# Kernel tuning notes

Hardware: AMD Instinct MI355X
Metric: run time of the kernel (lower is better)

Reference implementation:

```python
import jax, jax.numpy as jnp
import numpy as np

N = 100000
E = 1280000
D = 64


def setup_inputs() -> dict:
    key = jax.random.key(0)
    k1, k2, k3, k4, k5, k6 = jax.random.split(key, 6)
    return {
        "x": jax.random.normal(k1, (N, D), dtype=jnp.float32),
        "w_src": jax.random.normal(k2, (D,), dtype=jnp.float32),
        "w_dst": jax.random.normal(k3, (D,), dtype=jnp.float32),
        "ew": jax.random.normal(k4, (E,), dtype=jnp.float32),
        "src_idx": jax.random.randint(k5, (E,), 0, N, dtype=jnp.int64),
        "dst_idx": jax.random.randint(k6, (E,), 0, N, dtype=jnp.int64),
    }


def reference(x, w_src, w_dst, ew, src_idx, dst_idx):
    # Per-node scalar scores: Linear(emb_dim, 1, bias=False)
    a_src = x @ w_src            # [N]
    a_dst = x @ w_dst            # [N]
    # Edge attention: tanh(a_src[u] + a_dst[v]) * ew  (u_add_v + tanh + scale)
    a = jnp.tanh(a_src[src_idx] + a_dst[dst_idx]) * ew   # [E]
    # Message = a_e * x[src_e]; reduce = scatter-sum over dst (u_mul_e + sum)
    m = a[:, None] * x[src_idx]                           # [E, D]
    h = jax.ops.segment_sum(m, dst_idx, num_segments=N)   # [N, D]
    return h
```

## Files before the change

kernel.cpp:

```cpp
#include <hip/hip_runtime.h>
#include <hip/hip_fp16.h>
#include <math.h>

#define DIM  64
#define SPAN 256
#define SPAN_SHIFT 8
#define NBIN 256
#define KMAX 512
#define CAP  6144

__global__ void score_kernel(const float* __restrict__ x,
                             const float* __restrict__ w_src,
                             const float* __restrict__ w_dst,
                             float* __restrict__ a_src,
                             float* __restrict__ a_dst,
                             __half* __restrict__ xh,
                             int N) {
    int gid  = blockIdx.x * blockDim.x + threadIdx.x;
    int node = gid >> 6;
    int lane = threadIdx.x & 63;
    if (node >= N) return;
    float xv = x[(size_t)node * DIM + lane];
    xh[(size_t)node * DIM + lane] = __float2half_rn(xv);
    float s1 = xv * w_src[lane];
    float s2 = xv * w_dst[lane];
    #pragma unroll
    for (int off = 32; off > 0; off >>= 1) {
        s1 += __shfl_down(s1, off, 64);
        s2 += __shfl_down(s2, off, 64);
    }
    if (lane == 0) {
        a_src[node] = s1;
        a_dst[node] = s2;
    }
}

__global__ __launch_bounds__(1024) void hist_coarse(
        const int* __restrict__ dst, int* __restrict__ cnt,
        int E, int N, int K) {
    __shared__ int lh[KMAX];
    int tid = threadIdx.x;
    for (int j = tid; j < K; j += blockDim.x) lh[j] = 0;
    __syncthreads();
    for (int base = blockIdx.x * 1024; base < E; base += NBIN * 1024) {
        int e = base + tid;
        if (e < E) {
            unsigned t = (unsigned)dst[e];
            if (t >= (unsigned)N) t = 0;
            atomicAdd(&lh[t >> SPAN_SHIFT], 1);
        }
    }
    __syncthreads();
    for (int j = tid; j < K; j += blockDim.x)
        cnt[j * NBIN + blockIdx.x] = lh[j];
}

__global__ void scan_part(const int* __restrict__ cnt, int* __restrict__ offs,
                          int* __restrict__ bsum, int N) {
    __shared__ int buf[2][256];
    int tid = threadIdx.x;
    int i = blockIdx.x * 256 + tid;
    int v = (i < N) ? cnt[i] : 0;
    int sel = 0;
    buf[0][tid] = v;
    __syncthreads();
    for (int off = 1; off < 256; off <<= 1) {
        int nsel = sel ^ 1;
        buf[nsel][tid] = buf[sel][tid] + ((tid >= off) ? buf[sel][tid - off] : 0);
        __syncthreads();
        sel = nsel;
    }
    if (i < N) offs[i] = buf[sel][tid] - v;
    if (tid == 255) bsum[blockIdx.x] = buf[sel][255];
}

__global__ void scan_top(int* __restrict__ bsum, int* __restrict__ offs,
                         int NB, int N) {
    __shared__ int buf[2][512];
    int tid = threadIdx.x;
    int v = (tid < NB) ? bsum[tid] : 0;
    int sel = 0;
    buf[0][tid] = v;
    __syncthreads();
    for (int off = 1; off < 512; off <<= 1) {
        int nsel = sel ^ 1;
        buf[nsel][tid] = buf[sel][tid] + ((tid >= off) ? buf[sel][tid - off] : 0);
        __syncthreads();
        sel = nsel;
    }
    if (tid < NB) bsum[tid] = buf[sel][tid] - v;
    if (tid == 511) offs[N] = buf[sel][511];
}

__global__ __launch_bounds__(1024) void binpass_kernel(
        const float* __restrict__ ew,
        const int* __restrict__ src_idx,
        const int* __restrict__ dst_idx,
        const float* __restrict__ a_src,
        const float* __restrict__ a_dst,
        const int* __restrict__ moffs,
        const int* __restrict__ bsum,
        unsigned long long* __restrict__ pay,
        int E, int N, int K) {
    __shared__ int lcur[KMAX];
    int tid = threadIdx.x;
    for (int j = tid; j < K; j += blockDim.x) {
        int i = j * NBIN + blockIdx.x;
        lcur[j] = moffs[i] + bsum[i >> 8];
    }
    __syncthreads();
    for (int base = blockIdx.x * 1024; base < E; base += NBIN * 1024) {
        int e = base + tid;
        if (e < E) {
            unsigned s = (unsigned)src_idx[e];
            unsigned t = (unsigned)dst_idx[e];
            if (s >= (unsigned)N) s = 0;
            if (t >= (unsigned)N) t = 0;
            float a = tanhf(a_src[s] + a_dst[t]) * ew[e];
            int bk = (int)(t >> SPAN_SHIFT);
            int pos = atomicAdd(&lcur[bk], 1);
            unsigned rec = (s << 8) | (t & (SPAN - 1u));
            pay[pos] = ((unsigned long long)rec << 32) |
                       (unsigned long long)__float_as_uint(a);
        }
    }
}

__global__ __launch_bounds__(1024) void sort_gather_kernel(
        const __half* __restrict__ xh,
        const float* __restrict__ x32,
        const unsigned long long* __restrict__ pay,
        const int* __restrict__ moffs,
        const int* __restrict__ bsum,
        float* __restrict__ h,
        int N, int K, int E) {
    __shared__ unsigned long long srec[CAP];
    __shared__ unsigned short sidx[CAP];
    __shared__ int hcnt[SPAN];
    __shared__ int hoff[2][SPAN];
    __shared__ int lcur[SPAN];
    __shared__ int nstart[SPAN];
    int tid = threadIdx.x;
    int b   = blockIdx.x;
    int i0 = b * NBIN;
    int bstart = moffs[i0] + bsum[i0 >> 8];
    int bend;
    if (b == K - 1) bend = E;
    else { int i1 = (b + 1) * NBIN; bend = moffs[i1] + bsum[i1 >> 8]; }
    int cnt = bend - bstart;

    if (cnt <= CAP) {
        if (tid < SPAN) hcnt[tid] = 0;
        __syncthreads();
        for (int i = tid; i < cnt; i += 1024) {
            unsigned long long r = pay[bstart + i];
            srec[i] = r;
            atomicAdd(&hcnt[(int)((r >> 32) & (SPAN - 1u))], 1);
        }
        __syncthreads();
        int sel = 0;
        if (tid < SPAN) hoff[0][tid] = hcnt[tid];
        __syncthreads();
        for (int off = 1; off < SPAN; off <<= 1) {
            int nsel = sel ^ 1;
            if (tid < SPAN)
                hoff[nsel][tid] = hoff[sel][tid] +
                                  ((tid >= off) ? hoff[sel][tid - off] : 0);
            __syncthreads();
            sel = nsel;
        }
        if (tid < SPAN) {
            int excl = hoff[sel][tid] - hcnt[tid];
            nstart[tid] = excl;
            lcur[tid]   = excl;
        }
        __syncthreads();
        for (int i = tid; i < cnt; i += 1024) {
            unsigned long long r = srec[i];
            int d = (int)((r >> 32) & (SPAN - 1u));
            int pos = atomicAdd(&lcur[d], 1);
            sidx[pos] = (unsigned short)i;
        }
        __syncthreads();
        int lane = tid & 63;
        int wave = tid >> 6;
        int grp  = lane >> 4;
        int sub  = lane & 15;
        for (int d0 = (wave << 2); d0 < SPAN; d0 += 64) {
            int d = d0 + grp;
            int node = b * SPAN + d;
            int p  = nstart[d];
            int pe = p + hcnt[d];
            if (node >= N) pe = p;
            float ax = 0.f, ay = 0.f, az = 0.f, aw = 0.f;
            while (p + 4 <= pe) {
                unsigned long long r0 = srec[sidx[p]];
                unsigned long long r1 = srec[sidx[p + 1]];
                unsigned long long r2 = srec[sidx[p + 2]];
                unsigned long long r3 = srec[sidx[p + 3]];
                p += 4;
                unsigned s0 = (unsigned)(r0 >> 40); if (s0 >= (unsigned)N) s0 = 0;
                unsigned s1 = (unsigned)(r1 >> 40); if (s1 >= (unsigned)N) s1 = 0;
                unsigned s2 = (unsigned)(r2 >> 40); if (s2 >= (unsigned)N) s2 = 0;
                unsigned s3 = (unsigned)(r3 >> 40); if (s3 >= (unsigned)N) s3 = 0;
                uint2 v0 = *(const uint2*)(xh + (size_t)s0 * DIM + (sub << 2));
                uint2 v1 = *(const uint2*)(xh + (size_t)s1 * DIM + (sub << 2));
                uint2 v2 = *(const uint2*)(xh + (size_t)s2 * DIM + (sub << 2));
                uint2 v3 = *(const uint2*)(xh + (size_t)s3 * DIM + (sub << 2));
                float a0 = __uint_as_float((unsigned)r0);
                float a1 = __uint_as_float((unsigned)r1);
                float a2 = __uint_as_float((unsigned)r2);
                float a3 = __uint_as_float((unsigned)r3);
                float2 lo0 = __half22float2(*(const __half2*)&v0.x);
                float2 hi0 = __half22float2(*(const __half2*)&v0.y);
                float2 lo1 = __half22float2(*(const __half2*)&v1.x);
                float2 hi1 = __half22float2(*(const __half2*)&v1.y);
                float2 lo2 = __half22float2(*(const __half2*)&v2.x);
                float2 hi2 = __half22float2(*(const __half2*)&v2.y);
                float2 lo3 = __half22float2(*(const __half2*)&v3.x);
                float2 hi3 = __half22float2(*(const __half2*)&v3.y);
                ax = fmaf(a0, lo0.x, ax); ay = fmaf(a0, lo0.y, ay);
                az = fmaf(a0, hi0.x, az); aw = fmaf(a0, hi0.y, aw);
                ax = fmaf(a1, lo1.x, ax); ay = fmaf(a1, lo1.y, ay);
                az = fmaf(a1, hi1.x, az); aw = fmaf(a1, hi1.y, aw);
                ax = fmaf(a2, lo2.x, ax); ay = fmaf(a2, lo2.y, ay);
                az = fmaf(a2, hi2.x, az); aw = fmaf(a2, hi2.y, aw);
                ax = fmaf(a3, lo3.x, ax); ay = fmaf(a3, lo3.y, ay);
                az = fmaf(a3, hi3.x, az); aw = fmaf(a3, hi3.y, aw);
            }
            if (p < pe) {
                int q1 = p + 1, q2 = p + 2, q3 = p + 3;
                unsigned long long r0 = srec[sidx[p]];
                unsigned long long r1 = (q1 < pe) ? srec[sidx[q1]] : 0ULL;
                unsigned long long r2 = (q2 < pe) ? srec[sidx[q2]] : 0ULL;
                unsigned long long r3 = (q3 < pe) ? srec[sidx[q3]] : 0ULL;
                unsigned s0 = (unsigned)(r0 >> 40); if (s0 >= (unsigned)N) s0 = 0;
                unsigned s1 = (unsigned)(r1 >> 40); if (s1 >= (unsigned)N) s1 = 0;
                unsigned s2 = (unsigned)(r2 >> 40); if (s2 >= (unsigned)N) s2 = 0;
                unsigned s3 = (unsigned)(r3 >> 40); if (s3 >= (unsigned)N) s3 = 0;
                uint2 v0 = *(const uint2*)(xh + (size_t)s0 * DIM + (sub << 2));
                uint2 v1 = *(const uint2*)(xh + (size_t)s1 * DIM + (sub << 2));
                uint2 v2 = *(const uint2*)(xh + (size_t)s2 * DIM + (sub << 2));
                uint2 v3 = *(const uint2*)(xh + (size_t)s3 * DIM + (sub << 2));
                float a0 = __uint_as_float((unsigned)r0);
                float a1 = __uint_as_float((unsigned)r1);
                float a2 = __uint_as_float((unsigned)r2);
                float a3 = __uint_as_float((unsigned)r3);
                float2 lo0 = __half22float2(*(const __half2*)&v0.x);
                float2 hi0 = __half22float2(*(const __half2*)&v0.y);
                float2 lo1 = __half22float2(*(const __half2*)&v1.x);
                float2 hi1 = __half22float2(*(const __half2*)&v1.y);
                float2 lo2 = __half22float2(*(const __half2*)&v2.x);
                float2 hi2 = __half22float2(*(const __half2*)&v2.y);
                float2 lo3 = __half22float2(*(const __half2*)&v3.x);
                float2 hi3 = __half22float2(*(const __half2*)&v3.y);
                ax = fmaf(a0, lo0.x, ax); ay = fmaf(a0, lo0.y, ay);
                az = fmaf(a0, hi0.x, az); aw = fmaf(a0, hi0.y, aw);
                ax = fmaf(a1, lo1.x, ax); ay = fmaf(a1, lo1.y, ay);
                az = fmaf(a1, hi1.x, az); aw = fmaf(a1, hi1.y, aw);
                ax = fmaf(a2, lo2.x, ax); ay = fmaf(a2, lo2.y, ay);
                az = fmaf(a2, hi2.x, az); aw = fmaf(a2, hi2.y, aw);
                ax = fmaf(a3, lo3.x, ax); ay = fmaf(a3, lo3.y, ay);
                az = fmaf(a3, hi3.x, az); aw = fmaf(a3, hi3.y, aw);
            }
            if (node < N) {
                *(float4*)(h + (size_t)node * DIM + (sub << 2)) =
                    make_float4(ax, ay, az, aw);
            }
        }
    } else {
        for (int j = tid; j < SPAN * DIM; j += 1024) {
            int node = b * SPAN + (j >> 6);
            if (node < N) h[(size_t)node * DIM + (j & 63)] = 0.f;
        }
        __syncthreads();
        for (int i = tid; i < cnt; i += 1024) {
            unsigned long long r = pay[bstart + i];
            unsigned s = (unsigned)(r >> 40);
            if (s >= (unsigned)N) s = 0;
            int node = b * SPAN + (int)((r >> 32) & (SPAN - 1u));
            float a = __uint_as_float((unsigned)r);
            if (node < N)
                for (int k = 0; k < DIM; ++k)
                    atomicAdd(&h[(size_t)node * DIM + k],
                              a * x32[(size_t)s * DIM + k]);
        }
    }
}

__global__ void zero_h_kernel(float* __restrict__ p, int n) {
    int i = blockIdx.x * blockDim.x + threadIdx.x;
    if (i < n) p[i] = 0.f;
}

__global__ void edge_kernel_atomic(const float* __restrict__ x,
                                   const float* __restrict__ ew,
                                   const int* __restrict__ src_idx,
                                   const int* __restrict__ dst_idx,
                                   const float* __restrict__ a_src,
                                   const float* __restrict__ a_dst,
                                   float* __restrict__ h,
                                   int E) {
    int gid  = blockIdx.x * blockDim.x + threadIdx.x;
    int e    = gid >> 6;
    int lane = threadIdx.x & 63;
    if (e >= E) return;
    int s = src_idx[e];
    int t = dst_idx[e];
    float a  = tanhf(a_src[s] + a_dst[t]) * ew[e];
    float xv = x[(size_t)s * DIM + lane];
    atomicAdd(&h[(size_t)t * DIM + lane], a * xv);
}

__global__ void score_only_kernel(const float* __restrict__ x,
                                  const float* __restrict__ w_src,
                                  const float* __restrict__ w_dst,
                                  float* __restrict__ a_src,
                                  float* __restrict__ a_dst,
                                  int N) {
    int gid  = blockIdx.x * blockDim.x + threadIdx.x;
    int node = gid >> 6;
    int lane = threadIdx.x & 63;
    if (node >= N) return;
    float xv = x[(size_t)node * DIM + lane];
    float s1 = xv * w_src[lane];
    float s2 = xv * w_dst[lane];
    #pragma unroll
    for (int off = 32; off > 0; off >>= 1) {
        s1 += __shfl_down(s1, off, 64);
        s2 += __shfl_down(s2, off, 64);
    }
    if (lane == 0) {
        a_src[node] = s1;
        a_dst[node] = s2;
    }
}

extern "C" void kernel_launch(void* const* d_in, const int* in_sizes, int n_in,
                              void* d_out, int out_size, void* d_ws, size_t ws_size,
                              hipStream_t stream) {
    const float* x     = (const float*)d_in[0];
    const float* w_src = (const float*)d_in[1];
    const float* w_dst = (const float*)d_in[2];
    const float* ew    = (const float*)d_in[3];
    const int*   src   = (const int*)d_in[4];
    const int*   dst   = (const int*)d_in[5];
    float* h = (float*)d_out;

    int N = in_sizes[0] / DIM;
    int E = in_sizes[3];

    int K    = (N + SPAN - 1) / SPAN;
    int Ntot = K * NBIN;
    int NBs  = (Ntot + 255) / 256;

    float* a_src  = (float*)d_ws;
    float* a_dst  = a_src + N;
    int*   moffs  = (int*)(a_dst + N);
    int*   bsum   = moffs + Ntot + 1;
    size_t head_bytes = ((size_t)(2 * N) + (size_t)Ntot + 1 + (size_t)NBs) * 4;
    size_t pay_off = (head_bytes + 15) & ~(size_t)15;
    unsigned long long* pay = (unsigned long long*)((char*)d_ws + pay_off);
    size_t xh_off = pay_off + (size_t)E * 8;
    __half* xh = (__half*)((char*)d_ws + xh_off);
    size_t need = xh_off + (size_t)N * DIM * 2;

    int score_blocks = (N + 3) / 4;

    if (ws_size < need || K > KMAX || NBs > 512 || (N * DIM) % 2 != 0) {
        score_only_kernel<<<score_blocks, 256, 0, stream>>>(x, w_src, w_dst,
                                                            a_src, a_dst, N);
        int ob = (out_size + 255) / 256;
        zero_h_kernel<<<ob, 256, 0, stream>>>(h, out_size);
        int edge_blocks = (E + 3) / 4;
        edge_kernel_atomic<<<edge_blocks, 256, 0, stream>>>(x, ew, src, dst,
                                                            a_src, a_dst, h, E);
        return;
    }

    score_kernel<<<score_blocks, 256, 0, stream>>>(x, w_src, w_dst,
                                                   a_src, a_dst, xh, N);
    hist_coarse<<<NBIN, 1024, 0, stream>>>(dst, moffs, E, N, K);
    scan_part<<<NBs, 256, 0, stream>>>(moffs, moffs, bsum, Ntot);
    scan_top<<<1, 512, 0, stream>>>(bsum, moffs, NBs, Ntot);
    binpass_kernel<<<NBIN, 1024, 0, stream>>>(ew, src, dst, a_src, a_dst,
                                              moffs, bsum, pay, E, N, K);
    sort_gather_kernel<<<K, 1024, 0, stream>>>(xh, x, pay, moffs, bsum,
                                               h, N, K, E);
}
```

Before: 179.5 us.

## Fuse score, histogram, scan, binning and gather into one cooperative kernel

```diff
diff --git a/kernel.cpp b/kernel.cpp
--- a/kernel.cpp
+++ b/kernel.cpp
@@ -1,117 +1,114 @@
 #include <hip/hip_runtime.h>
+#include <hip/hip_cooperative_groups.h>
 #include <hip/hip_fp16.h>
 #include <math.h>
+
+namespace cg = cooperative_groups;
+typedef unsigned long long ull;
 
 #define DIM  64
 #define SPAN 256
 #define SPAN_SHIFT 8
-#define NBIN 256
 #define KMAX 512
 #define CAP  6144
-
-__global__ void score_kernel(const float* __restrict__ x,
-                             const float* __restrict__ w_src,
-                             const float* __restrict__ w_dst,
-                             float* __restrict__ a_src,
-                             float* __restrict__ a_dst,
-                             __half* __restrict__ xh,
-                             int N) {
-    int gid  = blockIdx.x * blockDim.x + threadIdx.x;
-    int node = gid >> 6;
-    int lane = threadIdx.x & 63;
-    if (node >= N) return;
-    float xv = x[(size_t)node * DIM + lane];
-    xh[(size_t)node * DIM + lane] = __float2half_rn(xv);
-    float s1 = xv * w_src[lane];
-    float s2 = xv * w_dst[lane];
-    #pragma unroll
-    for (int off = 32; off > 0; off >>= 1) {
-        s1 += __shfl_down(s1, off, 64);
-        s2 += __shfl_down(s2, off, 64);
-    }
-    if (lane == 0) {
-        a_src[node] = s1;
-        a_dst[node] = s2;
-    }
-}
-
-__global__ __launch_bounds__(1024) void hist_coarse(
-        const int* __restrict__ dst, int* __restrict__ cnt,
-        int E, int N, int K) {
-    __shared__ int lh[KMAX];
-    int tid = threadIdx.x;
-    for (int j = tid; j < K; j += blockDim.x) lh[j] = 0;
-    __syncthreads();
-    for (int base = blockIdx.x * 1024; base < E; base += NBIN * 1024) {
-        int e = base + tid;
-        if (e < E) {
-            unsigned t = (unsigned)dst[e];
-            if (t >= (unsigned)N) t = 0;
-            atomicAdd(&lh[t >> SPAN_SHIFT], 1);
-        }
-    }
-    __syncthreads();
-    for (int j = tid; j < K; j += blockDim.x)
-        cnt[j * NBIN + blockIdx.x] = lh[j];
-}
-
-__global__ void scan_part(const int* __restrict__ cnt, int* __restrict__ offs,
-                          int* __restrict__ bsum, int N) {
-    __shared__ int buf[2][256];
-    int tid = threadIdx.x;
-    int i = blockIdx.x * 256 + tid;
-    int v = (i < N) ? cnt[i] : 0;
-    int sel = 0;
-    buf[0][tid] = v;
-    __syncthreads();
-    for (int off = 1; off < 256; off <<= 1) {
-        int nsel = sel ^ 1;
-        buf[nsel][tid] = buf[sel][tid] + ((tid >= off) ? buf[sel][tid - off] : 0);
-        __syncthreads();
-        sel = nsel;
-    }
-    if (i < N) offs[i] = buf[sel][tid] - v;
-    if (tid == 255) bsum[blockIdx.x] = buf[sel][255];
-}
-
-__global__ void scan_top(int* __restrict__ bsum, int* __restrict__ offs,
-                         int NB, int N) {
-    __shared__ int buf[2][512];
-    int tid = threadIdx.x;
-    int v = (tid < NB) ? bsum[tid] : 0;
-    int sel = 0;
-    buf[0][tid] = v;
-    __syncthreads();
-    for (int off = 1; off < 512; off <<= 1) {
-        int nsel = sel ^ 1;
-        buf[nsel][tid] = buf[sel][tid] + ((tid >= off) ? buf[sel][tid - off] : 0);
-        __syncthreads();
-        sel = nsel;
-    }
-    if (tid < NB) bsum[tid] = buf[sel][tid] - v;
-    if (tid == 511) offs[N] = buf[sel][511];
-}
-
-__global__ __launch_bounds__(1024) void binpass_kernel(
+#define TPB  1024
+#define GRID 256
+
+#define SMEM_BYTES 66560
+
+__global__ __launch_bounds__(TPB) void fused_kernel(
+        const float* __restrict__ x,
+        const float* __restrict__ w_src,
+        const float* __restrict__ w_dst,
         const float* __restrict__ ew,
         const int* __restrict__ src_idx,
         const int* __restrict__ dst_idx,
-        const float* __restrict__ a_src,
-        const float* __restrict__ a_dst,
-        const int* __restrict__ moffs,
-        const int* __restrict__ bsum,
-        unsigned long long* __restrict__ pay,
-        int E, int N, int K) {
-    __shared__ int lcur[KMAX];
-    int tid = threadIdx.x;
-    for (int j = tid; j < K; j += blockDim.x) {
-        int i = j * NBIN + blockIdx.x;
-        lcur[j] = moffs[i] + bsum[i >> 8];
-    }
-    __syncthreads();
-    for (int base = blockIdx.x * 1024; base < E; base += NBIN * 1024) {
-        int e = base + tid;
-        if (e < E) {
+        float* __restrict__ a_src,
+        float* __restrict__ a_dst,
+        __half* __restrict__ xh,
+        int* __restrict__ moffs,
+        int* __restrict__ bsum,
+        ull* __restrict__ pay,
+        float* __restrict__ h,
+        int N, int E, int K, int NBs) {
+    cg::grid_group grid = cg::this_grid();
+    const int G   = gridDim.x;
+    const int b   = blockIdx.x;
+    const int tid = threadIdx.x;
+    __shared__ __align__(16) char smem[SMEM_BYTES];
+
+    {
+        int* lh = (int*)smem;
+        for (int j = tid; j < K; j += TPB) lh[j] = 0;
+        __syncthreads();
+        int lane = tid & 63;
+        for (int node = b * 16 + (tid >> 6); node < N; node += G * 16) {
+            float xv = x[(size_t)node * DIM + lane];
+            xh[(size_t)node * DIM + lane] = __float2half_rn(xv);
+            float s1 = xv * w_src[lane];
+            float s2 = xv * w_dst[lane];
+            #pragma unroll
+            for (int off = 32; off > 0; off >>= 1) {
+                s1 += __shfl_down(s1, off, 64);
+                s2 += __shfl_down(s2, off, 64);
+            }
+            if (lane == 0) { a_src[node] = s1; a_dst[node] = s2; }
+        }
+        for (int e = b * TPB + tid; e < E; e += G * TPB) {
+            unsigned t = (unsigned)dst_idx[e];
+            if (t >= (unsigned)N) t = 0;
+            atomicAdd(&lh[t >> SPAN_SHIFT], 1);
+        }
+        __syncthreads();
+        for (int j = tid; j < K; j += TPB) moffs[j * G + b] = lh[j];
+    }
+    grid.sync();
+
+    int Ntot = K * G;
+    if (b < NBs) {
+        int* buf = (int*)smem;
+        int i = b * TPB + tid;
+        int v = (i < Ntot) ? moffs[i] : 0;
+        int sel = 0;
+        buf[tid] = v;
+        __syncthreads();
+        for (int off = 1; off < TPB; off <<= 1) {
+            int nsel = sel ^ 1;
+            int add = (tid >= off) ? buf[sel * TPB + tid - off] : 0;
+            buf[nsel * TPB + tid] = buf[sel * TPB + tid] + add;
+            __syncthreads();
+            sel = nsel;
+        }
+        if (i < Ntot) moffs[i] = buf[sel * TPB + tid] - v;
+        if (tid == TPB - 1) bsum[b] = buf[sel * TPB + tid];
+    }
+    grid.sync();
+
+    if (b == 0) {
+        int* buf = (int*)smem;
+        int v = (tid < NBs) ? bsum[tid] : 0;
+        int sel = 0;
+        buf[tid] = v;
+        __syncthreads();
+        for (int off = 1; off < TPB; off <<= 1) {
+            int nsel = sel ^ 1;
+            int add = (tid >= off) ? buf[sel * TPB + tid - off] : 0;
+            buf[nsel * TPB + tid] = buf[sel * TPB + tid] + add;
+            __syncthreads();
+            sel = nsel;
+        }
+        if (tid < NBs) bsum[tid] = buf[sel * TPB + tid] - v;
+    }
+    grid.sync();
+
+    {
+        int* lcur = (int*)smem;
+        for (int j = tid; j < K; j += TPB) {
+            int i = j * G + b;
+            lcur[j] = moffs[i] + bsum[i >> 10];
+        }
+        __syncthreads();
+        for (int e = b * TPB + tid; e < E; e += G * TPB) {
             unsigned s = (unsigned)src_idx[e];
             unsigned t = (unsigned)dst_idx[e];
             if (s >= (unsigned)N) s = 0;
@@ -120,170 +117,163 @@
             int bk = (int)(t >> SPAN_SHIFT);
             int pos = atomicAdd(&lcur[bk], 1);
             unsigned rec = (s << 8) | (t & (SPAN - 1u));
-            pay[pos] = ((unsigned long long)rec << 32) |
-                       (unsigned long long)__float_as_uint(a);
-        }
-    }
-}
-
-__global__ __launch_bounds__(1024) void sort_gather_kernel(
-        const __half* __restrict__ xh,
-        const float* __restrict__ x32,
-        const unsigned long long* __restrict__ pay,
-        const int* __restrict__ moffs,
-        const int* __restrict__ bsum,
-        float* __restrict__ h,
-        int N, int K, int E) {
-    __shared__ unsigned long long srec[CAP];
-    __shared__ unsigned short sidx[CAP];
-    __shared__ int hcnt[SPAN];
-    __shared__ int hoff[2][SPAN];
-    __shared__ int lcur[SPAN];
-    __shared__ int nstart[SPAN];
-    int tid = threadIdx.x;
-    int b   = blockIdx.x;
-    int i0 = b * NBIN;
-    int bstart = moffs[i0] + bsum[i0 >> 8];
-    int bend;
-    if (b == K - 1) bend = E;
-    else { int i1 = (b + 1) * NBIN; bend = moffs[i1] + bsum[i1 >> 8]; }
-    int cnt = bend - bstart;
-
-    if (cnt <= CAP) {
-        if (tid < SPAN) hcnt[tid] = 0;
-        __syncthreads();
-        for (int i = tid; i < cnt; i += 1024) {
-            unsigned long long r = pay[bstart + i];
-            srec[i] = r;
-            atomicAdd(&hcnt[(int)((r >> 32) & (SPAN - 1u))], 1);
-        }
-        __syncthreads();
-        int sel = 0;
-        if (tid < SPAN) hoff[0][tid] = hcnt[tid];
-        __syncthreads();
-        for (int off = 1; off < SPAN; off <<= 1) {
-            int nsel = sel ^ 1;
-            if (tid < SPAN)
-                hoff[nsel][tid] = hoff[sel][tid] +
-                                  ((tid >= off) ? hoff[sel][tid - off] : 0);
-            __syncthreads();
-            sel = nsel;
-        }
-        if (tid < SPAN) {
-            int excl = hoff[sel][tid] - hcnt[tid];
-            nstart[tid] = excl;
-            lcur[tid]   = excl;
-        }
-        __syncthreads();
-        for (int i = tid; i < cnt; i += 1024) {
-            unsigned long long r = srec[i];
-            int d = (int)((r >> 32) & (SPAN - 1u));
-            int pos = atomicAdd(&lcur[d], 1);
-            sidx[pos] = (unsigned short)i;
-        }
-        __syncthreads();
-        int lane = tid & 63;
-        int wave = tid >> 6;
-        int grp  = lane >> 4;
-        int sub  = lane & 15;
-        for (int d0 = (wave << 2); d0 < SPAN; d0 += 64) {
-            int d = d0 + grp;
-            int node = b * SPAN + d;
-            int p  = nstart[d];
-            int pe = p + hcnt[d];
-            if (node >= N) pe = p;
-            float ax = 0.f, ay = 0.f, az = 0.f, aw = 0.f;
-            while (p + 4 <= pe) {
-                unsigned long long r0 = srec[sidx[p]];
-                unsigned long long r1 = srec[sidx[p + 1]];
-                unsigned long long r2 = srec[sidx[p + 2]];
-                unsigned long long r3 = srec[sidx[p + 3]];
-                p += 4;
-                unsigned s0 = (unsigned)(r0 >> 40); if (s0 >= (unsigned)N) s0 = 0;
-                unsigned s1 = (unsigned)(r1 >> 40); if (s1 >= (unsigned)N) s1 = 0;
-                unsigned s2 = (unsigned)(r2 >> 40); if (s2 >= (unsigned)N) s2 = 0;
-                unsigned s3 = (unsigned)(r3 >> 40); if (s3 >= (unsigned)N) s3 = 0;
-                uint2 v0 = *(const uint2*)(xh + (size_t)s0 * DIM + (sub << 2));
-                uint2 v1 = *(const uint2*)(xh + (size_t)s1 * DIM + (sub << 2));
-                uint2 v2 = *(const uint2*)(xh + (size_t)s2 * DIM + (sub << 2));
-                uint2 v3 = *(const uint2*)(xh + (size_t)s3 * DIM + (sub << 2));
-                float a0 = __uint_as_float((unsigned)r0);
-                float a1 = __uint_as_float((unsigned)r1);
-                float a2 = __uint_as_float((unsigned)r2);
-                float a3 = __uint_as_float((unsigned)r3);
-                float2 lo0 = __half22float2(*(const __half2*)&v0.x);
-                float2 hi0 = __half22float2(*(const __half2*)&v0.y);
-                float2 lo1 = __half22float2(*(const __half2*)&v1.x);
-                float2 hi1 = __half22float2(*(const __half2*)&v1.y);
-                float2 lo2 = __half22float2(*(const __half2*)&v2.x);
-                float2 hi2 = __half22float2(*(const __half2*)&v2.y);
-                float2 lo3 = __half22float2(*(const __half2*)&v3.x);
-                float2 hi3 = __half22float2(*(const __half2*)&v3.y);
-                ax = fmaf(a0, lo0.x, ax); ay = fmaf(a0, lo0.y, ay);
-                az = fmaf(a0, hi0.x, az); aw = fmaf(a0, hi0.y, aw);
-                ax = fmaf(a1, lo1.x, ax); ay = fmaf(a1, lo1.y, ay);
-                az = fmaf(a1, hi1.x, az); aw = fmaf(a1, hi1.y, aw);
-                ax = fmaf(a2, lo2.x, ax); ay = fmaf(a2, lo2.y, ay);
-                az = fmaf(a2, hi2.x, az); aw = fmaf(a2, hi2.y, aw);
-                ax = fmaf(a3, lo3.x, ax); ay = fmaf(a3, lo3.y, ay);
-                az = fmaf(a3, hi3.x, az); aw = fmaf(a3, hi3.y, aw);
-            }
-            if (p < pe) {
-                int q1 = p + 1, q2 = p + 2, q3 = p + 3;
-                unsigned long long r0 = srec[sidx[p]];
-                unsigned long long r1 = (q1 < pe) ? srec[sidx[q1]] : 0ULL;
-                unsigned long long r2 = (q2 < pe) ? srec[sidx[q2]] : 0ULL;
-                unsigned long long r3 = (q3 < pe) ? srec[sidx[q3]] : 0ULL;
-                unsigned s0 = (unsigned)(r0 >> 40); if (s0 >= (unsigned)N) s0 = 0;
-                unsigned s1 = (unsigned)(r1 >> 40); if (s1 >= (unsigned)N) s1 = 0;
-                unsigned s2 = (unsigned)(r2 >> 40); if (s2 >= (unsigned)N) s2 = 0;
-                unsigned s3 = (unsigned)(r3 >> 40); if (s3 >= (unsigned)N) s3 = 0;
-                uint2 v0 = *(const uint2*)(xh + (size_t)s0 * DIM + (sub << 2));
-                uint2 v1 = *(const uint2*)(xh + (size_t)s1 * DIM + (sub << 2));
-                uint2 v2 = *(const uint2*)(xh + (size_t)s2 * DIM + (sub << 2));
-                uint2 v3 = *(const uint2*)(xh + (size_t)s3 * DIM + (sub << 2));
-                float a0 = __uint_as_float((unsigned)r0);
-                float a1 = __uint_as_float((unsigned)r1);
-                float a2 = __uint_as_float((unsigned)r2);
-                float a3 = __uint_as_float((unsigned)r3);
-                float2 lo0 = __half22float2(*(const __half2*)&v0.x);
-                float2 hi0 = __half22float2(*(const __half2*)&v0.y);
-                float2 lo1 = __half22float2(*(const __half2*)&v1.x);
-                float2 hi1 = __half22float2(*(const __half2*)&v1.y);
-                float2 lo2 = __half22float2(*(const __half2*)&v2.x);
-                float2 hi2 = __half22float2(*(const __half2*)&v2.y);
-                float2 lo3 = __half22float2(*(const __half2*)&v3.x);
-                float2 hi3 = __half22float2(*(const __half2*)&v3.y);
-                ax = fmaf(a0, lo0.x, ax); ay = fmaf(a0, lo0.y, ay);
-                az = fmaf(a0, hi0.x, az); aw = fmaf(a0, hi0.y, aw);
-                ax = fmaf(a1, lo1.x, ax); ay = fmaf(a1, lo1.y, ay);
-                az = fmaf(a1, hi1.x, az); aw = fmaf(a1, hi1.y, aw);
-                ax = fmaf(a2, lo2.x, ax); ay = fmaf(a2, lo2.y, ay);
-                az = fmaf(a2, hi2.x, az); aw = fmaf(a2, hi2.y, aw);
-                ax = fmaf(a3, lo3.x, ax); ay = fmaf(a3, lo3.y, ay);
-                az = fmaf(a3, hi3.x, az); aw = fmaf(a3, hi3.y, aw);
-            }
-            if (node < N) {
-                *(float4*)(h + (size_t)node * DIM + (sub << 2)) =
-                    make_float4(ax, ay, az, aw);
-            }
-        }
-    } else {
-        for (int j = tid; j < SPAN * DIM; j += 1024) {
-            int node = b * SPAN + (j >> 6);
-            if (node < N) h[(size_t)node * DIM + (j & 63)] = 0.f;
-        }
-        __syncthreads();
-        for (int i = tid; i < cnt; i += 1024) {
-            unsigned long long r = pay[bstart + i];
-            unsigned s = (unsigned)(r >> 40);
-            if (s >= (unsigned)N) s = 0;
-            int node = b * SPAN + (int)((r >> 32) & (SPAN - 1u));
-            float a = __uint_as_float((unsigned)r);
-            if (node < N)
-                for (int k = 0; k < DIM; ++k)
-                    atomicAdd(&h[(size_t)node * DIM + k],
-                              a * x32[(size_t)s * DIM + k]);
+            pay[pos] = ((ull)rec << 32) | (ull)__float_as_uint(a);
+        }
+    }
+    grid.sync();
+
+    ull* srec            = (ull*)smem;
+    unsigned short* sidx = (unsigned short*)(smem + CAP * 8);
+    int* hcnt            = (int*)(smem + CAP * 8 + CAP * 2);
+    int* hoff            = (int*)(smem + CAP * 8 + CAP * 2 + SPAN * 4);
+    int* lcur4           = (int*)(smem + CAP * 8 + CAP * 2 + SPAN * 4 * 3);
+    int* nstart          = (int*)(smem + CAP * 8 + CAP * 2 + SPAN * 4 * 4);
+
+    for (int bkt = b; bkt < K; bkt += G) {
+        __syncthreads();
+        int i0 = bkt * G;
+        int bstart = moffs[i0] + bsum[i0 >> 10];
+        int bend;
+        if (bkt == K - 1) bend = E;
+        else { int i1 = (bkt + 1) * G; bend = moffs[i1] + bsum[i1 >> 10]; }
+        int cnt = bend - bstart;
+
+        if (cnt <= CAP) {
+            if (tid < SPAN) hcnt[tid] = 0;
+            __syncthreads();
+            for (int i = tid; i < cnt; i += TPB) {
+                ull r = pay[bstart + i];
+                srec[i] = r;
+                atomicAdd(&hcnt[(int)((r >> 32) & (SPAN - 1u))], 1);
+            }
+            __syncthreads();
+            int sel = 0;
+            if (tid < SPAN) hoff[tid] = hcnt[tid];
+            __syncthreads();
+            for (int off = 1; off < SPAN; off <<= 1) {
+                int nsel = sel ^ 1;
+                if (tid < SPAN)
+                    hoff[nsel * SPAN + tid] = hoff[sel * SPAN + tid] +
+                        ((tid >= off) ? hoff[sel * SPAN + tid - off] : 0);
+                __syncthreads();
+                sel = nsel;
+            }
+            if (tid < SPAN) {
+                int excl = hoff[sel * SPAN + tid] - hcnt[tid];
+                nstart[tid] = excl;
+                lcur4[tid]  = excl;
+            }
+            __syncthreads();
+            for (int i = tid; i < cnt; i += TPB) {
+                ull r = srec[i];
+                int d = (int)((r >> 32) & (SPAN - 1u));
+                int pos = atomicAdd(&lcur4[d], 1);
+                sidx[pos] = (unsigned short)i;
+            }
+            __syncthreads();
+            int lane = tid & 63;
+            int wave = tid >> 6;
+            int grp  = lane >> 4;
+            int sub  = lane & 15;
+            for (int d0 = (wave << 2); d0 < SPAN; d0 += 64) {
+                int d = d0 + grp;
+                int node = bkt * SPAN + d;
+                int p  = nstart[d];
+                int pe = p + hcnt[d];
+                if (node >= N) pe = p;
+                float ax = 0.f, ay = 0.f, az = 0.f, aw = 0.f;
+                while (p + 4 <= pe) {
+                    ull r0 = srec[sidx[p]];
+                    ull r1 = srec[sidx[p + 1]];
+                    ull r2 = srec[sidx[p + 2]];
+                    ull r3 = srec[sidx[p + 3]];
+                    p += 4;
+                    unsigned s0 = (unsigned)(r0 >> 40); if (s0 >= (unsigned)N) s0 = 0;
+                    unsigned s1 = (unsigned)(r1 >> 40); if (s1 >= (unsigned)N) s1 = 0;
+                    unsigned s2 = (unsigned)(r2 >> 40); if (s2 >= (unsigned)N) s2 = 0;
+                    unsigned s3 = (unsigned)(r3 >> 40); if (s3 >= (unsigned)N) s3 = 0;
+                    uint2 v0 = *(const uint2*)(xh + (size_t)s0 * DIM + (sub << 2));
+                    uint2 v1 = *(const uint2*)(xh + (size_t)s1 * DIM + (sub << 2));
+                    uint2 v2 = *(const uint2*)(xh + (size_t)s2 * DIM + (sub << 2));
+                    uint2 v3 = *(const uint2*)(xh + (size_t)s3 * DIM + (sub << 2));
+                    float a0 = __uint_as_float((unsigned)r0);
+                    float a1 = __uint_as_float((unsigned)r1);
+                    float a2 = __uint_as_float((unsigned)r2);
+                    float a3 = __uint_as_float((unsigned)r3);
+                    float2 lo0 = __half22float2(*(const __half2*)&v0.x);
+                    float2 hi0 = __half22float2(*(const __half2*)&v0.y);
+                    float2 lo1 = __half22float2(*(const __half2*)&v1.x);
+                    float2 hi1 = __half22float2(*(const __half2*)&v1.y);
+                    float2 lo2 = __half22float2(*(const __half2*)&v2.x);
+                    float2 hi2 = __half22float2(*(const __half2*)&v2.y);
+                    float2 lo3 = __half22float2(*(const __half2*)&v3.x);
+                    float2 hi3 = __half22float2(*(const __half2*)&v3.y);
+                    ax = fmaf(a0, lo0.x, ax); ay = fmaf(a0, lo0.y, ay);
+                    az = fmaf(a0, hi0.x, az); aw = fmaf(a0, hi0.y, aw);
+                    ax = fmaf(a1, lo1.x, ax); ay = fmaf(a1, lo1.y, ay);
+                    az = fmaf(a1, hi1.x, az); aw = fmaf(a1, hi1.y, aw);
+                    ax = fmaf(a2, lo2.x, ax); ay = fmaf(a2, lo2.y, ay);
+                    az = fmaf(a2, hi2.x, az); aw = fmaf(a2, hi2.y, aw);
+                    ax = fmaf(a3, lo3.x, ax); ay = fmaf(a3, lo3.y, ay);
+                    az = fmaf(a3, hi3.x, az); aw = fmaf(a3, hi3.y, aw);
+                }
+                if (p < pe) {
+                    int q1 = p + 1, q2 = p + 2, q3 = p + 3;
+                    ull r0 = srec[sidx[p]];
+                    ull r1 = (q1 < pe) ? srec[sidx[q1]] : 0ULL;
+                    ull r2 = (q2 < pe) ? srec[sidx[q2]] : 0ULL;
+                    ull r3 = (q3 < pe) ? srec[sidx[q3]] : 0ULL;
+                    unsigned s0 = (unsigned)(r0 >> 40); if (s0 >= (unsigned)N) s0 = 0;
+                    unsigned s1 = (unsigned)(r1 >> 40); if (s1 >= (unsigned)N) s1 = 0;
+                    unsigned s2 = (unsigned)(r2 >> 40); if (s2 >= (unsigned)N) s2 = 0;
+                    unsigned s3 = (unsigned)(r3 >> 40); if (s3 >= (unsigned)N) s3 = 0;
+                    uint2 v0 = *(const uint2*)(xh + (size_t)s0 * DIM + (sub << 2));
+                    uint2 v1 = *(const uint2*)(xh + (size_t)s1 * DIM + (sub << 2));
+                    uint2 v2 = *(const uint2*)(xh + (size_t)s2 * DIM + (sub << 2));
+                    uint2 v3 = *(const uint2*)(xh + (size_t)s3 * DIM + (sub << 2));
+                    float a0 = __uint_as_float((unsigned)r0);
+                    float a1 = __uint_as_float((unsigned)r1);
+                    float a2 = __uint_as_float((unsigned)r2);
+                    float a3 = __uint_as_float((unsigned)r3);
+                    float2 lo0 = __half22float2(*(const __half2*)&v0.x);
+                    float2 hi0 = __half22float2(*(const __half2*)&v0.y);
+                    float2 lo1 = __half22float2(*(const __half2*)&v1.x);
+                    float2 hi1 = __half22float2(*(const __half2*)&v1.y);
+                    float2 lo2 = __half22float2(*(const __half2*)&v2.x);
+                    float2 hi2 = __half22float2(*(const __half2*)&v2.y);
+                    float2 lo3 = __half22float2(*(const __half2*)&v3.x);
+                    float2 hi3 = __half22float2(*(const __half2*)&v3.y);
+                    ax = fmaf(a0, lo0.x, ax); ay = fmaf(a0, lo0.y, ay);
+                    az = fmaf(a0, hi0.x, az); aw = fmaf(a0, hi0.y, aw);
+                    ax = fmaf(a1, lo1.x, ax); ay = fmaf(a1, lo1.y, ay);
+                    az = fmaf(a1, hi1.x, az); aw = fmaf(a1, hi1.y, aw);
+                    ax = fmaf(a2, lo2.x, ax); ay = fmaf(a2, lo2.y, ay);
+                    az = fmaf(a2, hi2.x, az); aw = fmaf(a2, hi2.y, aw);
+                    ax = fmaf(a3, lo3.x, ax); ay = fmaf(a3, lo3.y, ay);
+                    az = fmaf(a3, hi3.x, az); aw = fmaf(a3, hi3.y, aw);
+                }
+                if (node < N) {
+                    *(float4*)(h + (size_t)node * DIM + (sub << 2)) =
+                        make_float4(ax, ay, az, aw);
+                }
+            }
+        } else {
+            for (int j = tid; j < SPAN * DIM; j += TPB) {
+                int node = bkt * SPAN + (j >> 6);
+                if (node < N) h[(size_t)node * DIM + (j & 63)] = 0.f;
+            }
+            __syncthreads();
+            for (int i = tid; i < cnt; i += TPB) {
+                ull r = pay[bstart + i];
+                unsigned s = (unsigned)(r >> 40);
+                if (s >= (unsigned)N) s = 0;
+                int node = bkt * SPAN + (int)((r >> 32) & (SPAN - 1u));
+                float a = __uint_as_float((unsigned)r);
+                if (node < N)
+                    for (int k = 0; k < DIM; ++k)
+                        atomicAdd(&h[(size_t)node * DIM + k],
+                                  a * x[(size_t)s * DIM + k]);
+            }
         }
     }
 }
@@ -336,6 +326,21 @@
     }
 }
 
+static void run_fallback(const float* x, const float* w_src,
+                         const float* w_dst, const float* ew,
+                         const int* src, const int* dst,
+                         float* a_src, float* a_dst, float* h,
+                         int N, int E, int out_size, hipStream_t stream) {
+    int score_blocks = (N + 3) / 4;
+    score_only_kernel<<<score_blocks, 256, 0, stream>>>(x, w_src, w_dst,
+                                                        a_src, a_dst, N);
+    int ob = (out_size + 255) / 256;
+    zero_h_kernel<<<ob, 256, 0, stream>>>(h, out_size);
+    int edge_blocks = (E + 3) / 4;
+    edge_kernel_atomic<<<edge_blocks, 256, 0, stream>>>(x, ew, src, dst,
+                                                        a_src, a_dst, h, E);
+}
+
 extern "C" void kernel_launch(void* const* d_in, const int* in_sizes, int n_in,
                               void* d_out, int out_size, void* d_ws, size_t ws_size,
                               hipStream_t stream) {
@@ -351,40 +356,40 @@
     int E = in_sizes[3];
 
     int K    = (N + SPAN - 1) / SPAN;
-    int Ntot = K * NBIN;
-    int NBs  = (Ntot + 255) / 256;
+    int G    = GRID;
+    int Ntot = K * G;
+    int NBs  = (Ntot + TPB - 1) / TPB;
 
     float* a_src  = (float*)d_ws;
     float* a_dst  = a_src + N;
     int*   moffs  = (int*)(a_dst + N);
-    int*   bsum   = moffs + Ntot + 1;
-    size_t head_bytes = ((size_t)(2 * N) + (size_t)Ntot + 1 + (size_t)NBs) * 4;
+    int*   bsum   = moffs + Ntot;
+    size_t head_bytes = ((size_t)(2 * N) + (size_t)Ntot + (size_t)NBs) * 4;
     size_t pay_off = (head_bytes + 15) & ~(size_t)15;
-    unsigned long long* pay = (unsigned long long*)((char*)d_ws + pay_off);
+    ull* pay = (ull*)((char*)d_ws + pay_off);
     size_t xh_off = pay_off + (size_t)E * 8;
     __half* xh = (__half*)((char*)d_ws + xh_off);
     size_t need = xh_off + (size_t)N * DIM * 2;
 
-    int score_blocks = (N + 3) / 4;
-
-    if (ws_size < need || K > KMAX || NBs > 512 || (N * DIM) % 2 != 0) {
-        score_only_kernel<<<score_blocks, 256, 0, stream>>>(x, w_src, w_dst,
-                                                            a_src, a_dst, N);
-        int ob = (out_size + 255) / 256;
-        zero_h_kernel<<<ob, 256, 0, stream>>>(h, out_size);
-        int edge_blocks = (E + 3) / 4;
-        edge_kernel_atomic<<<edge_blocks, 256, 0, stream>>>(x, ew, src, dst,
-                                                            a_src, a_dst, h, E);
+    if (ws_size < need || K > KMAX || K < 1 || NBs > G ||
+        (N * DIM) % 2 != 0) {
+        run_fallback(x, w_src, w_dst, ew, src, dst, a_src, a_dst, h,
+                     N, E, out_size, stream);
         return;
     }
 
-    score_kernel<<<score_blocks, 256, 0, stream>>>(x, w_src, w_dst,
-                                                   a_src, a_dst, xh, N);
-    hist_coarse<<<NBIN, 1024, 0, stream>>>(dst, moffs, E, N, K);
-    scan_part<<<NBs, 256, 0, stream>>>(moffs, moffs, bsum, Ntot);
-    scan_top<<<1, 512, 0, stream>>>(bsum, moffs, NBs, Ntot);
-    binpass_kernel<<<NBIN, 1024, 0, stream>>>(ew, src, dst, a_src, a_dst,
-                                              moffs, bsum, pay, E, N, K);
-    sort_gather_kernel<<<K, 1024, 0, stream>>>(xh, x, pay, moffs, bsum,
-                                               h, N, K, E);
-}
+    void* args[] = {
+        (void*)&x, (void*)&w_src, (void*)&w_dst, (void*)&ew,
+        (void*)&src, (void*)&dst,
+        (void*)&a_src, (void*)&a_dst, (void*)&xh,
+        (void*)&moffs, (void*)&bsum, (void*)&pay, (void*)&h,
+        (void*)&N, (void*)&E, (void*)&K, (void*)&NBs
+    };
+    hipError_t err = hipLaunchCooperativeKernel((const void*)fused_kernel,
+                                                dim3(G), dim3(TPB), args, 0,
+                                                stream);
+    if (err != hipSuccess) {
+        run_fallback(x, w_src, w_dst, ew, src, dst, a_src, a_dst, h,
+                     N, E, out_size, stream);
+    }
+}
```

New measurement: 313.7 us. +74.7%, slower.

## Replace per-block bucket offsets with global atomic bucket cursors

Applied to the files above, without the earlier changes.

```diff
diff --git a/kernel.cpp b/kernel.cpp
--- a/kernel.cpp
+++ b/kernel.cpp
@@ -2,10 +2,11 @@
 #include <hip/hip_fp16.h>
 #include <math.h>
 
+typedef unsigned long long ull;
+
 #define DIM  64
 #define SPAN 256
 #define SPAN_SHIFT 8
-#define NBIN 256
 #define KMAX 512
 #define CAP  6144
 
@@ -15,7 +16,11 @@
                              float* __restrict__ a_src,
                              float* __restrict__ a_dst,
                              __half* __restrict__ xh,
-                             int N) {
+                             int* __restrict__ gcnt,
+                             int N, int K) {
+    if (blockIdx.x == 0) {
+        for (int j = threadIdx.x; j < K; j += blockDim.x) gcnt[j] = 0;
+    }
     int gid  = blockIdx.x * blockDim.x + threadIdx.x;
     int node = gid >> 6;
     int lane = threadIdx.x & 63;
@@ -35,50 +40,44 @@
     }
 }
 
-__global__ __launch_bounds__(1024) void hist_coarse(
-        const int* __restrict__ dst, int* __restrict__ cnt,
+__global__ __launch_bounds__(1024) void hist_kernel(
+        const int* __restrict__ dst, int* __restrict__ gcnt,
         int E, int N, int K) {
     __shared__ int lh[KMAX];
     int tid = threadIdx.x;
     for (int j = tid; j < K; j += blockDim.x) lh[j] = 0;
     __syncthreads();
-    for (int base = blockIdx.x * 1024; base < E; base += NBIN * 1024) {
-        int e = base + tid;
-        if (e < E) {
-            unsigned t = (unsigned)dst[e];
-            if (t >= (unsigned)N) t = 0;
-            atomicAdd(&lh[t >> SPAN_SHIFT], 1);
-        }
+    int gtid   = blockIdx.x * blockDim.x + tid;
+    int stride = gridDim.x * blockDim.x;
+    int EV = E >> 2;
+    const int4* dst4 = (const int4*)dst;
+    for (int i = gtid; i < EV; i += stride) {
+        int4 t4 = dst4[i];
+        unsigned t0 = (unsigned)t4.x; if (t0 >= (unsigned)N) t0 = 0;
+        unsigned t1 = (unsigned)t4.y; if (t1 >= (unsigned)N) t1 = 0;
+        unsigned t2 = (unsigned)t4.z; if (t2 >= (unsigned)N) t2 = 0;
+        unsigned t3 = (unsigned)t4.w; if (t3 >= (unsigned)N) t3 = 0;
+        atomicAdd(&lh[t0 >> SPAN_SHIFT], 1);
+        atomicAdd(&lh[t1 >> SPAN_SHIFT], 1);
+        atomicAdd(&lh[t2 >> SPAN_SHIFT], 1);
+        atomicAdd(&lh[t3 >> SPAN_SHIFT], 1);
+    }
+    for (int e = (EV << 2) + gtid; e < E; e += stride) {
+        unsigned t = (unsigned)dst[e];
+        if (t >= (unsigned)N) t = 0;
+        atomicAdd(&lh[t >> SPAN_SHIFT], 1);
     }
     __syncthreads();
     for (int j = tid; j < K; j += blockDim.x)
-        cnt[j * NBIN + blockIdx.x] = lh[j];
-}
-
-__global__ void scan_part(const int* __restrict__ cnt, int* __restrict__ offs,
-                          int* __restrict__ bsum, int N) {
-    __shared__ int buf[2][256];
-    int tid = threadIdx.x;
-    int i = blockIdx.x * 256 + tid;
-    int v = (i < N) ? cnt[i] : 0;
-    int sel = 0;
-    buf[0][tid] = v;
-    __syncthreads();
-    for (int off = 1; off < 256; off <<= 1) {
-        int nsel = sel ^ 1;
-        buf[nsel][tid] = buf[sel][tid] + ((tid >= off) ? buf[sel][tid - off] : 0);
-        __syncthreads();
-        sel = nsel;
-    }
-    if (i < N) offs[i] = buf[sel][tid] - v;
-    if (tid == 255) bsum[blockIdx.x] = buf[sel][255];
-}
-
-__global__ void scan_top(int* __restrict__ bsum, int* __restrict__ offs,
-                         int NB, int N) {
+        if (lh[j]) atomicAdd(&gcnt[j], lh[j]);
+}
+
+__global__ __launch_bounds__(512) void scan_kernel(
+        const int* __restrict__ gcnt, int* __restrict__ gbase,
+        int* __restrict__ gcur, int K, int E) {
     __shared__ int buf[2][512];
     int tid = threadIdx.x;
-    int v = (tid < NB) ? bsum[tid] : 0;
+    int v = (tid < K) ? gcnt[tid] : 0;
     int sel = 0;
     buf[0][tid] = v;
     __syncthreads();
@@ -88,53 +87,60 @@
         __syncthreads();
         sel = nsel;
     }
-    if (tid < NB) bsum[tid] = buf[sel][tid] - v;
-    if (tid == 511) offs[N] = buf[sel][511];
-}
-
-__global__ __launch_bounds__(1024) void binpass_kernel(
+    if (tid < K) {
+        int excl = buf[sel][tid] - v;
+        gbase[tid] = excl;
+        gcur[tid]  = excl;
+    }
+    if (tid == 511) gbase[K] = E;
+}
+
+__global__ __launch_bounds__(256) void binpass_atomic(
         const float* __restrict__ ew,
         const int* __restrict__ src_idx,
         const int* __restrict__ dst_idx,
         const float* __restrict__ a_src,
         const float* __restrict__ a_dst,
-        const int* __restrict__ moffs,
-        const int* __restrict__ bsum,
-        unsigned long long* __restrict__ pay,
-        int E, int N, int K) {
-    __shared__ int lcur[KMAX];
-    int tid = threadIdx.x;
-    for (int j = tid; j < K; j += blockDim.x) {
-        int i = j * NBIN + blockIdx.x;
-        lcur[j] = moffs[i] + bsum[i >> 8];
-    }
-    __syncthreads();
-    for (int base = blockIdx.x * 1024; base < E; base += NBIN * 1024) {
-        int e = base + tid;
-        if (e < E) {
-            unsigned s = (unsigned)src_idx[e];
-            unsigned t = (unsigned)dst_idx[e];
-            if (s >= (unsigned)N) s = 0;
-            if (t >= (unsigned)N) t = 0;
-            float a = tanhf(a_src[s] + a_dst[t]) * ew[e];
-            int bk = (int)(t >> SPAN_SHIFT);
-            int pos = atomicAdd(&lcur[bk], 1);
-            unsigned rec = (s << 8) | (t & (SPAN - 1u));
-            pay[pos] = ((unsigned long long)rec << 32) |
-                       (unsigned long long)__float_as_uint(a);
-        }
+        int* __restrict__ gcur,
+        ull* __restrict__ pay,
+        int E, int N) {
+    int i  = blockIdx.x * blockDim.x + threadIdx.x;
+    int e0 = i << 1;
+    if (e0 >= E) return;
+    if (e0 + 1 < E) {
+        int2   s2 = ((const int2*)src_idx)[i];
+        int2   t2 = ((const int2*)dst_idx)[i];
+        float2 w2 = ((const float2*)ew)[i];
+        unsigned s0 = (unsigned)s2.x; if (s0 >= (unsigned)N) s0 = 0;
+        unsigned t0 = (unsigned)t2.x; if (t0 >= (unsigned)N) t0 = 0;
+        unsigned s1 = (unsigned)s2.y; if (s1 >= (unsigned)N) s1 = 0;
+        unsigned t1 = (unsigned)t2.y; if (t1 >= (unsigned)N) t1 = 0;
+        float a0 = tanhf(a_src[s0] + a_dst[t0]) * w2.x;
+        float a1 = tanhf(a_src[s1] + a_dst[t1]) * w2.y;
+        int p0 = atomicAdd(&gcur[t0 >> SPAN_SHIFT], 1);
+        int p1 = atomicAdd(&gcur[t1 >> SPAN_SHIFT], 1);
+        unsigned r0 = (s0 << 8) | (t0 & (SPAN - 1u));
+        unsigned r1 = (s1 << 8) | (t1 & (SPAN - 1u));
+        pay[p0] = ((ull)r0 << 32) | (ull)__float_as_uint(a0);
+        pay[p1] = ((ull)r1 << 32) | (ull)__float_as_uint(a1);
+    } else {
+        unsigned s0 = (unsigned)src_idx[e0]; if (s0 >= (unsigned)N) s0 = 0;
+        unsigned t0 = (unsigned)dst_idx[e0]; if (t0 >= (unsigned)N) t0 = 0;
+        float a0 = tanhf(a_src[s0] + a_dst[t0]) * ew[e0];
+        int p0 = atomicAdd(&gcur[t0 >> SPAN_SHIFT], 1);
+        unsigned r0 = (s0 << 8) | (t0 & (SPAN - 1u));
+        pay[p0] = ((ull)r0 << 32) | (ull)__float_as_uint(a0);
     }
 }
 
 __global__ __launch_bounds__(1024) void sort_gather_kernel(
         const __half* __restrict__ xh,
         const float* __restrict__ x32,
-        const unsigned long long* __restrict__ pay,
-        const int* __restrict__ moffs,
-        const int* __restrict__ bsum,
+        const ull* __restrict__ pay,
+        const int* __restrict__ gbase,
         float* __restrict__ h,
         int N, int K, int E) {
-    __shared__ unsigned long long srec[CAP];
+    __shared__ ull srec[CAP];
     __shared__ unsigned short sidx[CAP];
     __shared__ int hcnt[SPAN];
     __shared__ int hoff[2][SPAN];
@@ -142,18 +148,15 @@
     __shared__ int nstart[SPAN];
     int tid = threadIdx.x;
     int b   = blockIdx.x;
-    int i0 = b * NBIN;
-    int bstart = moffs[i0] + bsum[i0 >> 8];
-    int bend;
-    if (b == K - 1) bend = E;
-    else { int i1 = (b + 1) * NBIN; bend = moffs[i1] + bsum[i1 >> 8]; }
+    int bstart = gbase[b];
+    int bend   = gbase[b + 1];
     int cnt = bend - bstart;
 
     if (cnt <= CAP) {
         if (tid < SPAN) hcnt[tid] = 0;
         __syncthreads();
         for (int i = tid; i < cnt; i += 1024) {
-            unsigned long long r = pay[bstart + i];
+            ull r = pay[bstart + i];
             srec[i] = r;
             atomicAdd(&hcnt[(int)((r >> 32) & (SPAN - 1u))], 1);
         }
@@ -176,7 +179,7 @@
         }
         __syncthreads();
         for (int i = tid; i < cnt; i += 1024) {
-            unsigned long long r = srec[i];
+            ull r = srec[i];
             int d = (int)((r >> 32) & (SPAN - 1u));
             int pos = atomicAdd(&lcur[d], 1);
             sidx[pos] = (unsigned short)i;
@@ -194,10 +197,10 @@
             if (node >= N) pe = p;
             float ax = 0.f, ay = 0.f, az = 0.f, aw = 0.f;
             while (p + 4 <= pe) {
-                unsigned long long r0 = srec[sidx[p]];
-                unsigned long long r1 = srec[sidx[p + 1]];
-                unsigned long long r2 = srec[sidx[p + 2]];
-                unsigned long long r3 = srec[sidx[p + 3]];
+                ull r0 = srec[sidx[p]];
+                ull r1 = srec[sidx[p + 1]];
+                ull r2 = srec[sidx[p + 2]];
+                ull r3 = srec[sidx[p + 3]];
                 p += 4;
                 unsigned s0 = (unsigned)(r0 >> 40); if (s0 >= (unsigned)N) s0 = 0;
                 unsigned s1 = (unsigned)(r1 >> 40); if (s1 >= (unsigned)N) s1 = 0;
@@ -230,10 +233,10 @@
             }
             if (p < pe) {
                 int q1 = p + 1, q2 = p + 2, q3 = p + 3;
-                unsigned long long r0 = srec[sidx[p]];
-                unsigned long long r1 = (q1 < pe) ? srec[sidx[q1]] : 0ULL;
-                unsigned long long r2 = (q2 < pe) ? srec[sidx[q2]] : 0ULL;
-                unsigned long long r3 = (q3 < pe) ? srec[sidx[q3]] : 0ULL;
+                ull r0 = srec[sidx[p]];
+                ull r1 = (q1 < pe) ? srec[sidx[q1]] : 0ULL;
+                ull r2 = (q2 < pe) ? srec[sidx[q2]] : 0ULL;
+                ull r3 = (q3 < pe) ? srec[sidx[q3]] : 0ULL;
                 unsigned s0 = (unsigned)(r0 >> 40); if (s0 >= (unsigned)N) s0 = 0;
                 unsigned s1 = (unsigned)(r1 >> 40); if (s1 >= (unsigned)N) s1 = 0;
                 unsigned s2 = (unsigned)(r2 >> 40); if (s2 >= (unsigned)N) s2 = 0;
@@ -275,7 +278,7 @@
         }
         __syncthreads();
         for (int i = tid; i < cnt; i += 1024) {
-            unsigned long long r = pay[bstart + i];
+            ull r = pay[bstart + i];
             unsigned s = (unsigned)(r >> 40);
             if (s >= (unsigned)N) s = 0;
             int node = b * SPAN + (int)((r >> 32) & (SPAN - 1u));
@@ -350,24 +353,23 @@
     int N = in_sizes[0] / DIM;
     int E = in_sizes[3];
 
-    int K    = (N + SPAN - 1) / SPAN;
-    int Ntot = K * NBIN;
-    int NBs  = (Ntot + 255) / 256;
-
-    float* a_src  = (float*)d_ws;
-    float* a_dst  = a_src + N;
-    int*   moffs  = (int*)(a_dst + N);
-    int*   bsum   = moffs + Ntot + 1;
-    size_t head_bytes = ((size_t)(2 * N) + (size_t)Ntot + 1 + (size_t)NBs) * 4;
+    int K = (N + SPAN - 1) / SPAN;
+
+    float* a_src = (float*)d_ws;
+    float* a_dst = a_src + N;
+    int*   gcnt  = (int*)(a_dst + N);
+    int*   gbase = gcnt + K;
+    int*   gcur  = gbase + K + 1;
+    size_t head_bytes = ((size_t)(2 * N) + (size_t)(3 * K + 1)) * 4;
     size_t pay_off = (head_bytes + 15) & ~(size_t)15;
-    unsigned long long* pay = (unsigned long long*)((char*)d_ws + pay_off);
+    ull* pay = (ull*)((char*)d_ws + pay_off);
     size_t xh_off = pay_off + (size_t)E * 8;
     __half* xh = (__half*)((char*)d_ws + xh_off);
     size_t need = xh_off + (size_t)N * DIM * 2;
 
     int score_blocks = (N + 3) / 4;
 
-    if (ws_size < need || K > KMAX || NBs > 512 || (N * DIM) % 2 != 0) {
+    if (ws_size < need || K > KMAX || K < 1 || (N * DIM) % 2 != 0) {
         score_only_kernel<<<score_blocks, 256, 0, stream>>>(x, w_src, w_dst,
                                                             a_src, a_dst, N);
         int ob = (out_size + 255) / 256;
@@ -379,12 +381,13 @@
     }
 
     score_kernel<<<score_blocks, 256, 0, stream>>>(x, w_src, w_dst,
-                                                   a_src, a_dst, xh, N);
-    hist_coarse<<<NBIN, 1024, 0, stream>>>(dst, moffs, E, N, K);
-    scan_part<<<NBs, 256, 0, stream>>>(moffs, moffs, bsum, Ntot);
-    scan_top<<<1, 512, 0, stream>>>(bsum, moffs, NBs, Ntot);
-    binpass_kernel<<<NBIN, 1024, 0, stream>>>(ew, src, dst, a_src, a_dst,
-                                              moffs, bsum, pay, E, N, K);
-    sort_gather_kernel<<<K, 1024, 0, stream>>>(xh, x, pay, moffs, bsum,
+                                                   a_src, a_dst, xh,
+                                                   gcnt, N, K);
+    hist_kernel<<<256, 1024, 0, stream>>>(dst, gcnt, E, N, K);
+    scan_kernel<<<1, 512, 0, stream>>>(gcnt, gbase, gcur, K, E);
+    int bp_blocks = ((E + 1) / 2 + 255) / 256;
+    binpass_atomic<<<bp_blocks, 256, 0, stream>>>(ew, src, dst, a_src, a_dst,
+                                                  gcur, pay, E, N);
+    sort_gather_kernel<<<K, 1024, 0, stream>>>(xh, x, pay, gbase,
                                                h, N, K, E);
 }
```

Measured after the change: 602.5 us. 236% more time.
